# Optimization experiments

Measured on AMD Instinct MI355X. Metric: run time of the kernel, lower is better.

## Reference

```python
import jax, jax.numpy as jnp
import numpy as np

NEG_INF = -1e30  # stands in for float('-inf'); avoids nan in masked softmax edge cases


def setup_inputs() -> dict:
    key = jax.random.key(0)
    ks = jax.random.split(key, 6)
    B, N, MD, QD, AD = 64, 512, 1024, 1024, 1024
    stdv_m = 1.0 / np.sqrt(MD)
    stdv_q = 1.0 / np.sqrt(QD)
    stdv_a = 1.0 / np.sqrt(AD)
    return {
        "memory_values": jax.random.normal(ks[0], (B, N, MD), dtype=jnp.float32),
        "mask": jax.random.randint(ks[1], (B, N), 0, 2, dtype=jnp.int32),
        "query": jax.random.normal(ks[2], (B, QD), dtype=jnp.float32),
        "Wh": jax.random.uniform(ks[3], (MD, AD), jnp.float32, -stdv_m, stdv_m),
        "Ws": jax.random.uniform(ks[4], (QD, AD), jnp.float32, -stdv_q, stdv_q),
        "v": jax.random.uniform(ks[5], (AD, 1), jnp.float32, -stdv_a, stdv_a),
    }


def reference(memory_values, mask, query, Wh, Ws, v):
    # Et(i) = tanh(Hi*Wh + St*Ws) @ v ; At = softmax(Et) with masking
    tq = query @ Ws                                   # (B, AD)
    h = jnp.tanh(memory_values @ Wh + tq[:, None, :])  # (B, N, AD)
    logits = jnp.squeeze(h @ v, axis=-1)              # (B, N)

    maskf = mask.astype(logits.dtype)
    # no_cells[b] == 1 iff every cell in row b is masked out
    no_cells = jnp.prod(1.0 - maskf, axis=1, keepdims=True)  # (B, 1)
    suppress = jnp.where(maskf == 0, NEG_INF, 0.0)
    suppress = jnp.where(no_cells == 1.0, 0.0, suppress)
    weights = jax.nn.softmax(logits + suppress, axis=-1)
    weights = jnp.where(no_cells == 1.0, 0.0, weights)

    context = jnp.einsum("bn,bnd->bd", weights, memory_values)
    return context
```

## Files before the change

kernel.cpp:

```cpp
#include <hip/hip_runtime.h>
#include <cstdint>
#include <cstddef>

typedef float floatx4 __attribute__((ext_vector_type(4)));
typedef _Float16 half8_t __attribute__((ext_vector_type(8)));
typedef _Float16 half4_t __attribute__((ext_vector_type(4)));
typedef _Float16 half2_t __attribute__((ext_vector_type(2)));

#define AS1 __attribute__((address_space(1)))
#define AS3 __attribute__((address_space(3)))

__device__ __forceinline__ void glds16(const void* g, void* l) {
  __builtin_amdgcn_global_load_lds((const AS1 void*)g, (AS3 void*)l, 16, 0, 0);
}

__device__ __forceinline__ half2_t pkrtz(float a, float b) {
  return __builtin_bit_cast(half2_t, __builtin_amdgcn_cvt_pkrtz(a, b));
}

__device__ __forceinline__ float fast_tanh(float x) {
  float e2 = __expf(2.f * x);
  return 1.f - 2.f * __builtin_amdgcn_rcpf(e2 + 1.f);
}

__global__ __launch_bounds__(256) void k_prep(
    const float* __restrict__ mem, const float* __restrict__ Wh,
    const float* __restrict__ q, const float* __restrict__ Ws,
    _Float16* __restrict__ memh, _Float16* __restrict__ WhT,
    float* __restrict__ tqp) {
  __shared__ union {
    float t[64][65];
    struct { float qts[64][68]; float wss[64][68]; } k1;
  } sm;
  const int bx = blockIdx.x;
  const int tid = threadIdx.x;

  if (bx < 8192) {
    size_t base = ((size_t)bx << 12);
    #pragma unroll
    for (int p = 0; p < 4; ++p) {
      size_t i = base + (p << 10) + (tid << 2);
      floatx4 x = *(const floatx4*)(mem + i);
      half4_t h = {(_Float16)x[0], (_Float16)x[1], (_Float16)x[2], (_Float16)x[3]};
      *(half4_t*)(memh + i) = h;
    }
  } else if (bx < 8208) {
    const int n0 = (bx - 8192) << 6;
    const int c = tid & 63, rr = tid >> 6;
    for (int kt = 0; kt < 16; ++kt) {
      int k0 = kt << 6;
      #pragma unroll
      for (int i = 0; i < 16; ++i) {
        int r = (i << 2) + rr;
        sm.t[r][c] = Wh[(size_t)(k0 + r) * 1024 + n0 + c];
      }
      __syncthreads();
      #pragma unroll
      for (int i = 0; i < 16; ++i) {
        int r = (i << 2) + rr;
        WhT[(size_t)(n0 + r) * 1024 + k0 + c] = (_Float16)sm.t[c][r];
      }
      __syncthreads();
    }
  } else {
    const int bid2 = bx - 8208;
    const int db = (bid2 & 15) << 6, kb = (bid2 >> 4) << 6;
    for (int idx = tid; idx < 4096; idx += 256) {
      int b = idx >> 6, kk = idx & 63;
      sm.k1.qts[kk][b] = q[(b << 10) + kb + kk];
    }
    for (int idx = tid; idx < 4096; idx += 256) {
      int kk = idx >> 6, dd = idx & 63;
      sm.k1.wss[kk][dd] = Ws[(size_t)(kb + kk) * 1024 + db + dd];
    }
    __syncthreads();
    const int bq = tid >> 4, dq = tid & 15;
    floatx4 acc[4] = {{0.f, 0.f, 0.f, 0.f}, {0.f, 0.f, 0.f, 0.f},
                      {0.f, 0.f, 0.f, 0.f}, {0.f, 0.f, 0.f, 0.f}};
    for (int kk = 0; kk < 64; ++kk) {
      floatx4 wv = *(const floatx4*)&sm.k1.wss[kk][dq << 2];
      floatx4 qv = *(const floatx4*)&sm.k1.qts[kk][bq << 2];
      #pragma unroll
      for (int bb = 0; bb < 4; ++bb) acc[bb] += qv[bb] * wv;
    }
    #pragma unroll
    for (int bb = 0; bb < 4; ++bb) {
      int b = (bq << 2) + bb;
      *(floatx4*)(tqp + ((size_t)(bid2 >> 4) << 16) + (b << 10) + db + (dq << 2)) = acc[bb];
    }
  }
}

__global__ __launch_bounds__(256, 2) void k2_gemm_h(
    const _Float16* __restrict__ Ah, const _Float16* __restrict__ BT,
    const float* __restrict__ tqp, const float* __restrict__ v,
    float* __restrict__ partials) {
  __shared__ _Float16 As[128 * 32];
  __shared__ _Float16 Bs[128 * 32];
  const int bid = blockIdx.x;
  const int mtile = ((bid >> 6) << 3) | (bid & 7);
  const int nblk = (bid >> 3) & 7;
  const int m0 = mtile << 7, n0 = nblk << 7;
  const int tid = threadIdx.x;
  const int w = tid >> 6, lane = tid & 63;
  const int wm = w >> 1, wn = w & 1, quad = lane >> 4, l15 = lane & 15;

  const int b = m0 >> 9;
  const int colbase = n0 + (wn << 6) + l15;
  float tqv[4], vv[4];
  #pragma unroll
  for (int j = 0; j < 4; ++j) {
    int n = colbase + (j << 4);
    float s = 0.f;
    #pragma unroll
    for (int p = 0; p < 16; ++p) s += tqp[(p << 16) + (b << 10) + n];
    tqv[j] = s;
    vv[j] = v[n];
  }

  floatx4 acc[4][4];
  #pragma unroll
  for (int i = 0; i < 4; ++i)
    #pragma unroll
    for (int j = 0; j < 4; ++j) acc[i][j] = floatx4{0.f, 0.f, 0.f, 0.f};

  const _Float16 *gA[2], *gB[2];
  _Float16 *lA[2], *lB[2];
  #pragma unroll
  for (int t = 0; t < 2; ++t) {
    int L = (t << 8) + (w << 6) + lane;
    int row = L >> 2, jj = L & 3;
    int j = (jj - row - (row >> 2)) & 3;
    gA[t] = Ah + (size_t)(m0 + row) * 1024 + (j << 3);
    gB[t] = BT + (size_t)(n0 + row) * 1024 + (j << 3);
    lA[t] = As + (t << 11) + (w << 9);
    lB[t] = Bs + (t << 11) + (w << 9);
  }

  const half8_t *aaddr[4], *baddr[4];
  #pragma unroll
  for (int i = 0; i < 4; ++i) {
    int ar = (wm << 6) + (i << 4) + l15;
    aaddr[i] = (const half8_t*)(As + (ar << 5) + (((quad + ar + (ar >> 2)) & 3) << 3));
    int br = (wn << 6) + (i << 4) + l15;
    baddr[i] = (const half8_t*)(Bs + (br << 5) + (((quad + br + (br >> 2)) & 3) << 3));
  }

  for (int k0 = 0; k0 < 1024; k0 += 32) {
    __syncthreads();
    glds16(gA[0] + k0, lA[0]);
    glds16(gA[1] + k0, lA[1]);
    glds16(gB[0] + k0, lB[0]);
    glds16(gB[1] + k0, lB[1]);
    __syncthreads();
    half8_t af[4], bfr[4];
    #pragma unroll
    for (int i = 0; i < 4; ++i) af[i] = *aaddr[i];
    #pragma unroll
    for (int j = 0; j < 4; ++j) bfr[j] = *baddr[j];
    #pragma unroll
    for (int i = 0; i < 4; ++i)
      #pragma unroll
      for (int j = 0; j < 4; ++j)
        acc[i][j] = __builtin_amdgcn_mfma_f32_16x16x32_f16(af[i], bfr[j], acc[i][j], 0, 0, 0);
  }

  #pragma unroll
  for (int i = 0; i < 4; ++i) {
    #pragma unroll
    for (int r = 0; r < 4; ++r) {
      float s = 0.f;
      #pragma unroll
      for (int j = 0; j < 4; ++j) s += fast_tanh(acc[i][j][r] + tqv[j]) * vv[j];
      s += __shfl_xor(s, 1);
      s += __shfl_xor(s, 2);
      s += __shfl_xor(s, 4);
      s += __shfl_xor(s, 8);
      if (l15 == 0) {
        int m = m0 + (wm << 6) + (i << 4) + (quad << 2) + r;
        partials[m * 16 + (nblk << 1) + wn] = s;
      }
    }
  }
}

__global__ __launch_bounds__(512) void k3_softmax(const float* __restrict__ partials,
                                                  const int* __restrict__ mask,
                                                  float* __restrict__ weights) {
  int b = blockIdx.x;
  int n = threadIdx.x;
  int m = (b << 9) + n;
  float s = 0.f;
  #pragma unroll
  for (int i = 0; i < 16; ++i) s += partials[m * 16 + i];
  int mk = mask[m];
  float logit = mk ? s : -1e30f;
  __shared__ float red[8];
  float x = logit;
  #pragma unroll
  for (int off = 32; off > 0; off >>= 1) x = fmaxf(x, __shfl_xor(x, off));
  if ((n & 63) == 0) red[n >> 6] = x;
  __syncthreads();
  float mx = red[0];
  #pragma unroll
  for (int i = 1; i < 8; ++i) mx = fmaxf(mx, red[i]);
  float e = mk ? __expf(logit - mx) : 0.f;
  float ss = e;
  #pragma unroll
  for (int off = 32; off > 0; off >>= 1) ss += __shfl_xor(ss, off);
  __syncthreads();
  if ((n & 63) == 0) red[n >> 6] = ss;
  __syncthreads();
  float tot = 0.f;
  #pragma unroll
  for (int i = 0; i < 8; ++i) tot += red[i];
  weights[m] = (tot > 0.f) ? e / tot : 0.f;
}

__global__ __launch_bounds__(256) void k4_ctx_h(const _Float16* __restrict__ memh,
                                                const float* __restrict__ weights,
                                                float* __restrict__ ctxp) {
  int nc = blockIdx.x, b = blockIdx.y;
  int d = threadIdx.x << 2;
  float a0 = 0.f, a1 = 0.f, a2 = 0.f, a3 = 0.f;
  int nbase = nc << 6;
  for (int n = nbase; n < nbase + 64; ++n) {
    float wv = weights[(b << 9) + n];
    half4_t x = *(const half4_t*)(memh + ((size_t)((b << 9) + n) << 10) + d);
    a0 += wv * (float)x[0];
    a1 += wv * (float)x[1];
    a2 += wv * (float)x[2];
    a3 += wv * (float)x[3];
  }
  *(floatx4*)(ctxp + ((size_t)((b << 3) + nc) << 10) + d) = floatx4{a0, a1, a2, a3};
}

__global__ void k5_reduce8(const float* __restrict__ ctxp, float* __restrict__ out) {
  int i = (blockIdx.x << 8) + threadIdx.x;
  int b = i >> 10, d = i & 1023;
  float s = 0.f;
  #pragma unroll
  for (int cc = 0; cc < 8; ++cc) s += ctxp[((size_t)((b << 3) + cc) << 10) + d];
  out[i] = s;
}

__global__ void k0_transpose(const float* __restrict__ Wh, _Float16* __restrict__ WhT) {
  __shared__ float t[64][65];
  int k0 = blockIdx.y << 6, n0 = blockIdx.x << 6;
  int tx = threadIdx.x, ty = threadIdx.y;
  #pragma unroll
  for (int r = ty; r < 64; r += 4) t[r][tx] = Wh[(size_t)(k0 + r) * 1024 + n0 + tx];
  __syncthreads();
  #pragma unroll
  for (int r = ty; r < 64; r += 4)
    WhT[(size_t)(n0 + r) * 1024 + k0 + tx] = (_Float16)t[tx][r];
}

__global__ __launch_bounds__(256) void k1_tq(const float* __restrict__ q,
                                             const float* __restrict__ Ws,
                                             float* __restrict__ tq) {
  __shared__ float qs[1024];
  __shared__ float red[4][64];
  int b = blockIdx.y;
  int d0 = blockIdx.x << 6;
  int dl = threadIdx.x & 63, kg = threadIdx.x >> 6;
  for (int k = threadIdx.x; k < 1024; k += 256) qs[k] = q[(b << 10) + k];
  __syncthreads();
  float acc = 0.f;
  int kbase = kg << 8;
  #pragma unroll 8
  for (int k = 0; k < 256; ++k)
    acc += qs[kbase + k] * Ws[(size_t)(kbase + k) * 1024 + d0 + dl];
  red[kg][dl] = acc;
  __syncthreads();
  if (kg == 0)
    tq[(b << 10) + d0 + dl] = red[0][dl] + red[1][dl] + red[2][dl] + red[3][dl];
}

__global__ __launch_bounds__(256, 2) void k2_gemm_f32(
    const float* __restrict__ A, const _Float16* __restrict__ BT,
    const float* __restrict__ tq, const float* __restrict__ v,
    float* __restrict__ partials) {
  __shared__ float As[128 * 32];
  __shared__ _Float16 Bs[128 * 32];
  const int bid = blockIdx.x;
  const int mtile = ((bid >> 6) << 3) | (bid & 7);
  const int nblk = (bid >> 3) & 7;
  const int m0 = mtile << 7, n0 = nblk << 7;
  const int tid = threadIdx.x;
  const int w = tid >> 6, lane = tid & 63;
  const int wm = w >> 1, wn = w & 1, quad = lane >> 4, l15 = lane & 15;
  floatx4 acc[4][4];
  #pragma unroll
  for (int i = 0; i < 4; ++i)
    #pragma unroll
    for (int j = 0; j < 4; ++j) acc[i][j] = floatx4{0.f, 0.f, 0.f, 0.f};
  const float* gA[4];
  float* lA[4];
  #pragma unroll
  for (int t = 0; t < 4; ++t) {
    int L = (t << 8) + (w << 6) + lane;
    int row = L >> 3, jj = L & 7;
    int j = (jj - row) & 7;
    gA[t] = A + (size_t)(m0 + row) * 1024 + (j << 2);
    lA[t] = As + (t << 10) + (w << 8);
  }
  const _Float16* gB[2];
  _Float16* lB[2];
  #pragma unroll
  for (int t = 0; t < 2; ++t) {
    int L = (t << 8) + (w << 6) + lane;
    int row = L >> 2, jj = L & 3;
    int j = (jj - row - (row >> 2)) & 3;
    gB[t] = BT + (size_t)(n0 + row) * 1024 + (j << 3);
    lB[t] = Bs + (t << 11) + (w << 9);
  }
  const floatx4* aaddr[4][2];
  #pragma unroll
  for (int i = 0; i < 4; ++i) {
    int row = (wm << 6) + (i << 4) + l15;
    #pragma unroll
    for (int h = 0; h < 2; ++h) {
      int pos = ((quad << 1) + h + row) & 7;
      aaddr[i][h] = (const floatx4*)(As + (row << 5) + (pos << 2));
    }
  }
  const half8_t* baddr[4];
  #pragma unroll
  for (int j = 0; j < 4; ++j) {
    int row = (wn << 6) + (j << 4) + l15;
    int pos = (quad + row + (row >> 2)) & 3;
    baddr[j] = (const half8_t*)(Bs + (row << 5) + (pos << 3));
  }
  for (int k0 = 0; k0 < 1024; k0 += 32) {
    __syncthreads();
    glds16(gA[0] + k0, lA[0]);
    glds16(gA[1] + k0, lA[1]);
    glds16(gA[2] + k0, lA[2]);
    glds16(gA[3] + k0, lA[3]);
    glds16(gB[0] + k0, lB[0]);
    glds16(gB[1] + k0, lB[1]);
    __syncthreads();
    half8_t af[4], bfr[4];
    #pragma unroll
    for (int i = 0; i < 4; ++i) {
      floatx4 x = *aaddr[i][0], y = *aaddr[i][1];
      union { half2_t h2[4]; half8_t h8; } u;
      u.h2[0] = pkrtz(x[0], x[1]);
      u.h2[1] = pkrtz(x[2], x[3]);
      u.h2[2] = pkrtz(y[0], y[1]);
      u.h2[3] = pkrtz(y[2], y[3]);
      af[i] = u.h8;
    }
    #pragma unroll
    for (int j = 0; j < 4; ++j) bfr[j] = *baddr[j];
    #pragma unroll
    for (int i = 0; i < 4; ++i)
      #pragma unroll
      for (int j = 0; j < 4; ++j)
        acc[i][j] = __builtin_amdgcn_mfma_f32_16x16x32_f16(af[i], bfr[j], acc[i][j], 0, 0, 0);
  }
  const int b = m0 >> 9;
  const int colbase = n0 + (wn << 6) + l15;
  float tqv[4], vv[4];
  #pragma unroll
  for (int j = 0; j < 4; ++j) {
    int n = colbase + (j << 4);
    tqv[j] = tq[(b << 10) + n];
    vv[j] = v[n];
  }
  #pragma unroll
  for (int i = 0; i < 4; ++i) {
    #pragma unroll
    for (int r = 0; r < 4; ++r) {
      float s = 0.f;
      #pragma unroll
      for (int j = 0; j < 4; ++j) s += fast_tanh(acc[i][j][r] + tqv[j]) * vv[j];
      s += __shfl_xor(s, 1);
      s += __shfl_xor(s, 2);
      s += __shfl_xor(s, 4);
      s += __shfl_xor(s, 8);
      if (l15 == 0) {
        int m = m0 + (wm << 6) + (i << 4) + (quad << 2) + r;
        partials[m * 16 + (nblk << 1) + wn] = s;
      }
    }
  }
}

__global__ void k4_ctx_f32(const float* __restrict__ mem, const float* __restrict__ weights,
                           float* __restrict__ ctxp) {
  int nc = blockIdx.x, b = blockIdx.y;
  int d = threadIdx.x << 3;
  floatx4 a0 = {0.f, 0.f, 0.f, 0.f}, a1 = {0.f, 0.f, 0.f, 0.f};
  int nbase = nc << 6;
  for (int n = nbase; n < nbase + 64; ++n) {
    float wv = weights[(b << 9) + n];
    const floatx4* p = (const floatx4*)(mem + ((size_t)((b << 9) + n) << 10) + d);
    a0 += wv * p[0];
    a1 += wv * p[1];
  }
  floatx4* o = (floatx4*)(ctxp + ((size_t)((b << 3) + nc) << 10) + d);
  o[0] = a0;
  o[1] = a1;
}

extern "C" void kernel_launch(void* const* d_in, const int* in_sizes, int n_in,
                              void* d_out, int out_size, void* d_ws, size_t ws_size,
                              hipStream_t stream) {
  const float* mem = (const float*)d_in[0];
  const int* mask = (const int*)d_in[1];
  const float* query = (const float*)d_in[2];
  const float* Wh = (const float*)d_in[3];
  const float* Ws = (const float*)d_in[4];
  const float* v = (const float*)d_in[5];
  float* out = (float*)d_out;

  char* ws = (char*)d_ws;
  const size_t need16 = (73ull << 20);

  if (ws_size >= need16) {
    _Float16* memh = (_Float16*)ws;
    _Float16* WhT = (_Float16*)(ws + (64ull << 20));
    float* partials = (float*)(ws + (66ull << 20));
    float* tqp = (float*)(ws + (68ull << 20));
    float* ctxp = tqp;
    float* weights = (float*)(ws + (72ull << 20));

    k_prep<<<8464, 256, 0, stream>>>(mem, Wh, query, Ws, memh, WhT, tqp);
    k2_gemm_h<<<2048, 256, 0, stream>>>(memh, WhT, tqp, v, partials);
    k3_softmax<<<64, 512, 0, stream>>>(partials, mask, weights);
    k4_ctx_h<<<dim3(8, 64), 256, 0, stream>>>(memh, weights, ctxp);
    k5_reduce8<<<256, 256, 0, stream>>>(ctxp, out);
  } else {
    _Float16* WhT = (_Float16*)ws;
    float* partials = (float*)(ws + ((size_t)2 << 20));
    float* tq = (float*)(ws + ((size_t)4 << 20));
    float* weights = (float*)(ws + ((size_t)4 << 20) + (256 << 10));
    float* ctxp = (float*)(ws + ((size_t)9 << 19));

    k0_transpose<<<dim3(16, 16), dim3(64, 4), 0, stream>>>(Wh, WhT);
    k1_tq<<<dim3(16, 64), 256, 0, stream>>>(query, Ws, tq);
    k2_gemm_f32<<<2048, 256, 0, stream>>>(mem, WhT, tq, v, partials);
    k3_softmax<<<64, 512, 0, stream>>>(partials, mask, weights);
    k4_ctx_f32<<<dim3(8, 64), 128, 0, stream>>>(mem, weights, ctxp);
    k5_reduce8<<<256, 256, 0, stream>>>(ctxp, out);
  }
}
```

Before: 338.4 us.

## Fuse softmax and context reduction with atomics; spread Wh transpose over more blocks

Folds the softmax kernel and the split context reduction into a single kernel. Each block recomputes the row softmax from the partial logits and accumulates its context slice into the output with atomicAdd. The output is zeroed in the prep kernel. The Wh transpose now uses 256 blocks that each handle one tile, instead of 16 blocks that loop serially over tiles. The tq/v loads in the GEMM move after the main loop to ease register pressure. Together this cuts launches and intermediate buffers, at the cost of redundant softmax work across 8 blocks per row and float atomics that make the summation order nondeterministic.

```diff
diff --git a/kernel.cpp b/kernel.cpp
--- a/kernel.cpp
+++ b/kernel.cpp
@@ -27,7 +27,7 @@
     const float* __restrict__ mem, const float* __restrict__ Wh,
     const float* __restrict__ q, const float* __restrict__ Ws,
     _Float16* __restrict__ memh, _Float16* __restrict__ WhT,
-    float* __restrict__ tqp) {
+    float* __restrict__ tqp, float* __restrict__ outz) {
   __shared__ union {
     float t[64][65];
     struct { float qts[64][68]; float wss[64][68]; } k1;
@@ -44,26 +44,23 @@
       half4_t h = {(_Float16)x[0], (_Float16)x[1], (_Float16)x[2], (_Float16)x[3]};
       *(half4_t*)(memh + i) = h;
     }
-  } else if (bx < 8208) {
-    const int n0 = (bx - 8192) << 6;
+  } else if (bx < 8448) {
+    const int t2 = bx - 8192;
+    const int n0 = (t2 & 15) << 6, k0 = (t2 >> 4) << 6;
     const int c = tid & 63, rr = tid >> 6;
-    for (int kt = 0; kt < 16; ++kt) {
-      int k0 = kt << 6;
-      #pragma unroll
-      for (int i = 0; i < 16; ++i) {
-        int r = (i << 2) + rr;
-        sm.t[r][c] = Wh[(size_t)(k0 + r) * 1024 + n0 + c];
-      }
-      __syncthreads();
-      #pragma unroll
-      for (int i = 0; i < 16; ++i) {
-        int r = (i << 2) + rr;
-        WhT[(size_t)(n0 + r) * 1024 + k0 + c] = (_Float16)sm.t[c][r];
-      }
-      __syncthreads();
-    }
-  } else {
-    const int bid2 = bx - 8208;
+    #pragma unroll
+    for (int i = 0; i < 16; ++i) {
+      int r = (i << 2) + rr;
+      sm.t[r][c] = Wh[(size_t)(k0 + r) * 1024 + n0 + c];
+    }
+    __syncthreads();
+    #pragma unroll
+    for (int i = 0; i < 16; ++i) {
+      int r = (i << 2) + rr;
+      WhT[(size_t)(n0 + r) * 1024 + k0 + c] = (_Float16)sm.t[c][r];
+    }
+  } else if (bx < 8704) {
+    const int bid2 = bx - 8448;
     const int db = (bid2 & 15) << 6, kb = (bid2 >> 4) << 6;
     for (int idx = tid; idx < 4096; idx += 256) {
       int b = idx >> 6, kk = idx & 63;
@@ -88,6 +85,13 @@
       int b = (bq << 2) + bb;
       *(floatx4*)(tqp + ((size_t)(bid2 >> 4) << 16) + (b << 10) + db + (dq << 2)) = acc[bb];
     }
+  } else {
+    int base = ((bx - 8704) << 12) + (tid << 4);
+    floatx4 z = {0.f, 0.f, 0.f, 0.f};
+    *(floatx4*)(outz + base) = z;
+    *(floatx4*)(outz + base + 4) = z;
+    *(floatx4*)(outz + base + 8) = z;
+    *(floatx4*)(outz + base + 12) = z;
   }
 }
 
@@ -105,19 +109,6 @@
   const int w = tid >> 6, lane = tid & 63;
   const int wm = w >> 1, wn = w & 1, quad = lane >> 4, l15 = lane & 15;
 
-  const int b = m0 >> 9;
-  const int colbase = n0 + (wn << 6) + l15;
-  float tqv[4], vv[4];
-  #pragma unroll
-  for (int j = 0; j < 4; ++j) {
-    int n = colbase + (j << 4);
-    float s = 0.f;
-    #pragma unroll
-    for (int p = 0; p < 16; ++p) s += tqp[(p << 16) + (b << 10) + n];
-    tqv[j] = s;
-    vv[j] = v[n];
-  }
-
   floatx4 acc[4][4];
   #pragma unroll
   for (int i = 0; i < 4; ++i)
@@ -165,6 +156,17 @@
         acc[i][j] = __builtin_amdgcn_mfma_f32_16x16x32_f16(af[i], bfr[j], acc[i][j], 0, 0, 0);
   }
 
+  const int b = m0 >> 9;
+  const int colbase = n0 + (wn << 6) + l15;
+  float tqv[4], vv[4];
+  #pragma unroll
+  for (int j = 0; j < 4; ++j) {
+    int n = colbase + (j << 4);
+    float s = 0.f;
+    for (int p = 0; p < 16; ++p) s += tqp[(p << 16) + (b << 10) + n];
+    tqv[j] = s;
+    vv[j] = v[n];
+  }
   #pragma unroll
   for (int i = 0; i < 4; ++i) {
     #pragma unroll
@@ -184,64 +186,62 @@
   }
 }
 
-__global__ __launch_bounds__(512) void k3_softmax(const float* __restrict__ partials,
-                                                  const int* __restrict__ mask,
-                                                  float* __restrict__ weights) {
-  int b = blockIdx.x;
-  int n = threadIdx.x;
-  int m = (b << 9) + n;
-  float s = 0.f;
-  #pragma unroll
-  for (int i = 0; i < 16; ++i) s += partials[m * 16 + i];
-  int mk = mask[m];
-  float logit = mk ? s : -1e30f;
-  __shared__ float red[8];
-  float x = logit;
+__global__ __launch_bounds__(256) void k4_fused(const _Float16* __restrict__ memh,
+                                                const float* __restrict__ partials,
+                                                const int* __restrict__ mask,
+                                                float* __restrict__ out) {
+  __shared__ float wgt[512];
+  __shared__ float red[4];
+  const int nc = blockIdx.x, b = blockIdx.y;
+  const int tid = threadIdx.x;
+
+  float lg[2];
+  int mk[2];
+  #pragma unroll
+  for (int h = 0; h < 2; ++h) {
+    int n = (h << 8) + tid;
+    float s = 0.f;
+    #pragma unroll
+    for (int p = 0; p < 16; ++p) s += partials[(((b << 9) + n) << 4) + p];
+    mk[h] = mask[(b << 9) + n];
+    lg[h] = mk[h] ? s : -1e30f;
+  }
+  float x = fmaxf(lg[0], lg[1]);
   #pragma unroll
   for (int off = 32; off > 0; off >>= 1) x = fmaxf(x, __shfl_xor(x, off));
-  if ((n & 63) == 0) red[n >> 6] = x;
-  __syncthreads();
-  float mx = red[0];
-  #pragma unroll
-  for (int i = 1; i < 8; ++i) mx = fmaxf(mx, red[i]);
-  float e = mk ? __expf(logit - mx) : 0.f;
-  float ss = e;
+  if ((tid & 63) == 0) red[tid >> 6] = x;
+  __syncthreads();
+  float mx = fmaxf(fmaxf(red[0], red[1]), fmaxf(red[2], red[3]));
+  float e0 = mk[0] ? __expf(lg[0] - mx) : 0.f;
+  float e1 = mk[1] ? __expf(lg[1] - mx) : 0.f;
+  float ss = e0 + e1;
   #pragma unroll
   for (int off = 32; off > 0; off >>= 1) ss += __shfl_xor(ss, off);
   __syncthreads();
-  if ((n & 63) == 0) red[n >> 6] = ss;
-  __syncthreads();
-  float tot = 0.f;
-  #pragma unroll
-  for (int i = 0; i < 8; ++i) tot += red[i];
-  weights[m] = (tot > 0.f) ? e / tot : 0.f;
-}
-
-__global__ __launch_bounds__(256) void k4_ctx_h(const _Float16* __restrict__ memh,
-                                                const float* __restrict__ weights,
-                                                float* __restrict__ ctxp) {
-  int nc = blockIdx.x, b = blockIdx.y;
-  int d = threadIdx.x << 2;
+  if ((tid & 63) == 0) red[tid >> 6] = ss;
+  __syncthreads();
+  float tot = red[0] + red[1] + red[2] + red[3];
+  float inv = (tot > 0.f) ? 1.f / tot : 0.f;
+  wgt[tid] = e0 * inv;
+  wgt[tid + 256] = e1 * inv;
+  __syncthreads();
+
+  const int d = tid << 2;
   float a0 = 0.f, a1 = 0.f, a2 = 0.f, a3 = 0.f;
-  int nbase = nc << 6;
+  const int nbase = nc << 6;
   for (int n = nbase; n < nbase + 64; ++n) {
-    float wv = weights[(b << 9) + n];
-    half4_t x = *(const half4_t*)(memh + ((size_t)((b << 9) + n) << 10) + d);
-    a0 += wv * (float)x[0];
-    a1 += wv * (float)x[1];
-    a2 += wv * (float)x[2];
-    a3 += wv * (float)x[3];
-  }
-  *(floatx4*)(ctxp + ((size_t)((b << 3) + nc) << 10) + d) = floatx4{a0, a1, a2, a3};
-}
-
-__global__ void k5_reduce8(const float* __restrict__ ctxp, float* __restrict__ out) {
-  int i = (blockIdx.x << 8) + threadIdx.x;
-  int b = i >> 10, d = i & 1023;
-  float s = 0.f;
-  #pragma unroll
-  for (int cc = 0; cc < 8; ++cc) s += ctxp[((size_t)((b << 3) + cc) << 10) + d];
-  out[i] = s;
+    float wv = wgt[n];
+    half4_t xv = *(const half4_t*)(memh + ((size_t)((b << 9) + n) << 10) + d);
+    a0 += wv * (float)xv[0];
+    a1 += wv * (float)xv[1];
+    a2 += wv * (float)xv[2];
+    a3 += wv * (float)xv[3];
+  }
+  float* o = out + (b << 10) + d;
+  atomicAdd(o + 0, a0);
+  atomicAdd(o + 1, a1);
+  atomicAdd(o + 2, a2);
+  atomicAdd(o + 3, a3);
 }
 
 __global__ void k0_transpose(const float* __restrict__ Wh, _Float16* __restrict__ WhT) {
@@ -388,6 +388,39 @@
   }
 }
 
+__global__ __launch_bounds__(512) void k3_softmax(const float* __restrict__ partials,
+                                                  const int* __restrict__ mask,
+                                                  float* __restrict__ weights) {
+  int b = blockIdx.x;
+  int n = threadIdx.x;
+  int m = (b << 9) + n;
+  float s = 0.f;
+  #pragma unroll
+  for (int i = 0; i < 16; ++i) s += partials[m * 16 + i];
+  int mk = mask[m];
+  float logit = mk ? s : -1e30f;
+  __shared__ float red[8];
+  float x = logit;
+  #pragma unroll
+  for (int off = 32; off > 0; off >>= 1) x = fmaxf(x, __shfl_xor(x, off));
+  if ((n & 63) == 0) red[n >> 6] = x;
+  __syncthreads();
+  float mx = red[0];
+  #pragma unroll
+  for (int i = 1; i < 8; ++i) mx = fmaxf(mx, red[i]);
+  float e = mk ? __expf(logit - mx) : 0.f;
+  float ss = e;
+  #pragma unroll
+  for (int off = 32; off > 0; off >>= 1) ss += __shfl_xor(ss, off);
+  __syncthreads();
+  if ((n & 63) == 0) red[n >> 6] = ss;
+  __syncthreads();
+  float tot = 0.f;
+  #pragma unroll
+  for (int i = 0; i < 8; ++i) tot += red[i];
+  weights[m] = (tot > 0.f) ? e / tot : 0.f;
+}
+
 __global__ void k4_ctx_f32(const float* __restrict__ mem, const float* __restrict__ weights,
                            float* __restrict__ ctxp) {
   int nc = blockIdx.x, b = blockIdx.y;
@@ -405,6 +438,15 @@
   o[1] = a1;
 }
 
+__global__ void k5_reduce8(const float* __restrict__ ctxp, float* __restrict__ out) {
+  int i = (blockIdx.x << 8) + threadIdx.x;
+  int b = i >> 10, d = i & 1023;
+  float s = 0.f;
+  #pragma unroll
+  for (int cc = 0; cc < 8; ++cc) s += ctxp[((size_t)((b << 3) + cc) << 10) + d];
+  out[i] = s;
+}
+
 extern "C" void kernel_launch(void* const* d_in, const int* in_sizes, int n_in,
                               void* d_out, int out_size, void* d_ws, size_t ws_size,
                               hipStream_t stream) {
@@ -424,14 +466,10 @@
     _Float16* WhT = (_Float16*)(ws + (64ull << 20));
     float* partials = (float*)(ws + (66ull << 20));
     float* tqp = (float*)(ws + (68ull << 20));
-    float* ctxp = tqp;
-    float* weights = (float*)(ws + (72ull << 20));
-
-    k_prep<<<8464, 256, 0, stream>>>(mem, Wh, query, Ws, memh, WhT, tqp);
+
+    k_prep<<<8720, 256, 0, stream>>>(mem, Wh, query, Ws, memh, WhT, tqp, out);
     k2_gemm_h<<<2048, 256, 0, stream>>>(memh, WhT, tqp, v, partials);
-    k3_softmax<<<64, 512, 0, stream>>>(partials, mask, weights);
-    k4_ctx_h<<<dim3(8, 64), 256, 0, stream>>>(memh, weights, ctxp);
-    k5_reduce8<<<256, 256, 0, stream>>>(ctxp, out);
+    k4_fused<<<dim3(8, 64), 256, 0, stream>>>(memh, partials, mask, out);
   } else {
     _Float16* WhT = (_Float16*)ws;
     float* partials = (float*)(ws + ((size_t)2 << 20));
```

Result: slower. 348.3 us (+2.9%).
